# Performance work log

Measured on AMD Instinct MI355X. Metric: run time of the kernel, lower is better.

## Reference

```python
import jax, jax.numpy as jnp
import numpy as np
import math

N_QUBITS = 6
N_LAYERS = 3
OUT_DIM = 8
B = 131072
F = 24


def _gate_rx(a):
    # RX(a) = [[cos(a/2), -i sin(a/2)], [-i sin(a/2), cos(a/2)]]; a: scalar or [B]
    c = jnp.cos(a / 2).astype(jnp.complex64)
    s = (-1j * jnp.sin(a / 2)).astype(jnp.complex64)
    return jnp.stack([jnp.stack([c, s], -1), jnp.stack([s, c], -1)], -2)


def _gate_ry(a):
    c = jnp.cos(a / 2).astype(jnp.complex64)
    s = jnp.sin(a / 2).astype(jnp.complex64)
    return jnp.stack([jnp.stack([c, -s], -1), jnp.stack([s, c], -1)], -2)


def _gate_rz(a):
    # RZ(a) = diag(e^{-ia/2}, e^{ia/2})
    e = jnp.exp(-0.5j * a.astype(jnp.complex64))
    z = jnp.zeros_like(e)
    return jnp.stack([jnp.stack([e, z], -1), jnp.stack([z, jnp.conj(e)], -1)], -2)


def _apply_1q(state, gate, q, batched):
    # state: [B] + [2]*N_QUBITS ; gate: [2,2] or [B,2,2]
    s = jnp.moveaxis(state, 1 + q, 1)
    if batched:
        out = jnp.einsum('bij,bj...->bi...', gate, s)
    else:
        out = jnp.einsum('ij,bj...->bi...', gate, s)
    return jnp.moveaxis(out, 1, 1 + q)


def _apply_cnot(state, c, t):
    # flip target where control bit == 1
    cax = 1 + c
    s0 = jnp.take(state, 0, axis=cax)
    s1 = jnp.take(state, 1, axis=cax)
    tax = 1 + t if t < c else t  # control axis removed
    s1 = jnp.flip(s1, axis=tax)
    return jnp.stack([s0, s1], axis=cax)


def _circuit(x, theta):
    Bn = x.shape[0]
    # pooling branch of forward: chunks of size ceil(F/n_qubits)=4, mean each
    x_packed = x.reshape(Bn, N_QUBITS, F // N_QUBITS).mean(-1)
    angles = jnp.clip(x_packed, -6.0, 6.0) / 6.0 * math.pi  # [B, n_qubits]

    state = jnp.zeros((Bn,) + (2,) * N_QUBITS, dtype=jnp.complex64)
    state = state.at[(slice(None),) + (0,) * N_QUBITS].set(1.0)

    # angle encoding: RX(a_q), RZ(0.5*a_q) per qubit (batched gates)
    for q in range(N_QUBITS):
        state = _apply_1q(state, _gate_rx(angles[:, q]), q, batched=True)
        state = _apply_1q(state, _gate_rz(0.5 * angles[:, q]), q, batched=True)

    for l in range(N_LAYERS):
        for q in range(N_QUBITS - 1):
            state = _apply_cnot(state, q, q + 1)
        state = _apply_cnot(state, N_QUBITS - 1, 0)
        for q in range(N_QUBITS):
            state = _apply_1q(state, _gate_rx(theta[l, q, 0]), q, batched=False)
            state = _apply_1q(state, _gate_ry(theta[l, q, 1]), q, batched=False)
            state = _apply_1q(state, _gate_rz(theta[l, q, 2]), q, batched=False)

    probs = jnp.abs(state) ** 2  # real
    meas = []
    for k in range(OUT_DIM):
        q = k % N_QUBITS
        if k % 2 == 0:  # PauliZ
            pq = jnp.sum(probs, axis=tuple(a for a in range(1, N_QUBITS + 1) if a != 1 + q))
            meas.append(pq[:, 0] - pq[:, 1])
        else:  # PauliX: Re <psi| X_q |psi>
            flipped = jnp.flip(state, axis=1 + q)
            meas.append(jnp.real(jnp.sum(jnp.conj(state) * flipped, axis=tuple(range(1, N_QUBITS + 1)))))
    return jnp.stack(meas, axis=1).astype(jnp.float32)  # [B, out_dim]


def setup_inputs() -> dict:
    key = jax.random.key(0)
    k1, k2 = jax.random.split(key)
    x = jax.random.normal(k1, (B, F), dtype=jnp.float32)
    theta = jax.random.normal(k2, (N_LAYERS, N_QUBITS, 3), dtype=jnp.float32) * 0.1
    return {"x": x, "theta": theta}


def reference(x, theta):
    return _circuit(x, theta)
```

## Files before the change

### kernel.cpp

```cpp
#include <hip/hip_runtime.h>
#include <math.h>


__device__ __forceinline__ float2 pk_cmul(float2 g, float2 a) {
    float2 t;
    asm("v_pk_mul_f32 %0, %1, %2 op_sel:[0,0] op_sel_hi:[0,1]"
        : "=v"(t) : "v"(g), "v"(a));
    asm("v_pk_fma_f32 %0, %1, %2, %0 op_sel:[1,1,0] op_sel_hi:[1,0,1] neg_lo:[1,0,0]"
        : "+v"(t) : "v"(g), "v"(a));
    return t;
}
__device__ __forceinline__ float2 pk_cmac(float2 acc, float2 g, float2 a) {
    asm("v_pk_fma_f32 %0, %1, %2, %0 op_sel:[0,0,0] op_sel_hi:[0,1,1]"
        : "+v"(acc) : "v"(g), "v"(a));
    asm("v_pk_fma_f32 %0, %1, %2, %0 op_sel:[1,1,0] op_sel_hi:[1,0,1] neg_lo:[1,0,0]"
        : "+v"(acc) : "v"(g), "v"(a));
    return acc;
}
__device__ __forceinline__ float2 pk_sqacc(float2 acc, float2 a) {
    asm("v_pk_fma_f32 %0, %1, %1, %0" : "+v"(acc) : "v"(a));
    return acc;
}
__device__ __forceinline__ float2 pk_macv(float2 acc, float2 a, float2 b) {
    asm("v_pk_fma_f32 %0, %1, %2, %0" : "+v"(acc) : "v"(a), "v"(b));
    return acc;
}

__device__ __forceinline__ float xpair(float v) {
    return __int_as_float(__builtin_amdgcn_mov_dpp(__float_as_int(v), 0xB1, 0xF, 0xF, true));
}
__device__ __forceinline__ float2 xpair2(float2 v) {
    return make_float2(xpair(v.x), xpair(v.y));
}

template<int M>
__device__ __forceinline__ void apply1q(float2* st, float2 g00, float2 g01,
                                        float2 g10, float2 g11) {
#pragma unroll
    for (int j = 0; j < 32; ++j) {
        if (j & M) continue;
        float2 a = st[j], b = st[j + M];
        float2 na = pk_cmul(g00, a); na = pk_cmac(na, g01, b);
        float2 nb = pk_cmul(g10, a); nb = pk_cmac(nb, g11, b);
        st[j] = na; st[j + M] = nb;
    }
}

template<int MC, int MT>
__device__ __forceinline__ void cnot(float2* st) {
#pragma unroll
    for (int j = 0; j < 32; ++j) {
        if ((j & MC) && !(j & MT)) {
            float2 tmp = st[j]; st[j] = st[j + MT]; st[j + MT] = tmp;
        }
    }
}

struct cf { float r, i; };
__device__ __forceinline__ cf scmul(cf a, cf b) {
    return { fmaf(a.r, b.r, -a.i * b.i), fmaf(a.r, b.i, a.i * b.r) };
}

__global__ __launch_bounds__(256, 2) void qsim_kernel(
    const float* __restrict__ x, const float* __restrict__ theta,
    float* __restrict__ out) {
    __shared__ float2 gs[18 * 4];
    const int t = threadIdx.x;
    if (t < 18) {
        const float* th = theta + t * 3;
        float sx, cx, sy, cy, sz, cz;
        __sincosf(0.5f * th[0], &sx, &cx);
        __sincosf(0.5f * th[1], &sy, &cy);
        __sincosf(0.5f * th[2], &sz, &cz);
        cf m00 = {  cy * cx,  sy * sx };
        cf m01 = { -sy * cx, -cy * sx };
        cf m10 = {  sy * cx, -cy * sx };
        cf m11 = {  cy * cx, -sy * sx };
        cf e0 = { cz, -sz }, e1 = { cz, sz };
        cf g00 = scmul(e0, m00), g01 = scmul(e0, m01);
        cf g10 = scmul(e1, m10), g11 = scmul(e1, m11);
        float2* o = gs + t * 4;
        o[0] = make_float2(g00.r, g00.i);
        o[1] = make_float2(g01.r, g01.i);
        o[2] = make_float2(g10.r, g10.i);
        o[3] = make_float2(g11.r, g11.i);
    }
    __syncthreads();

    const int tg = blockIdx.x * 256 + t;
    const int b  = tg >> 1;
    const bool pb = (tg & 1) != 0;

    const float4* xv = reinterpret_cast<const float4*>(x + (size_t)b * 24);

    float2 st[32];
#pragma unroll
    for (int q = 0; q < 6; ++q) {
        float4 v = xv[q];
        float m = (v.x + v.y + v.z + v.w) * 0.25f;
        m = fminf(fmaxf(m, -6.0f), 6.0f);
        float a = m * 0.52359877559829887308f;
        float s2, c2, s4, c4;
        __sincosf(0.50f * a, &s2, &c2);
        __sincosf(0.25f * a, &s4, &c4);
        float2 v0 = make_float2(c4 * c2, -s4 * c2);
        float2 v1 = make_float2(s4 * s2, -c4 * s2);
        if (q == 0) {
            st[0] = pb ? v1 : v0;
        } else {
            const int mq = 32 >> q;
#pragma unroll
            for (int i = 0; i < 32; i += 2 * mq) {
                st[i + mq] = pk_cmul(st[i], v1);
                st[i]      = pk_cmul(st[i], v0);
            }
        }
    }

#pragma unroll 1
    for (int l = 0; l < 3; ++l) {
#pragma unroll
        for (int j = 0; j < 16; ++j) {
            float2 lo = st[j], hi = st[j + 16];
            st[j].x      = pb ? hi.x : lo.x;  st[j].y      = pb ? hi.y : lo.y;
            st[j + 16].x = pb ? lo.x : hi.x;  st[j + 16].y = pb ? lo.y : hi.y;
        }
        cnot<16, 8>(st);
        cnot< 8, 4>(st);
        cnot< 4, 2>(st);
        cnot< 2, 1>(st);
#pragma unroll
        for (int j = 1; j < 32; j += 2) st[j] = xpair2(st[j]);

        const float2* g = gs + l * 24;

        {
            float2 q00 = g[0], q01 = g[1], q10 = g[2], q11 = g[3];
            float2 gm, go;
            gm.x = pb ? q11.x : q00.x;  gm.y = pb ? q11.y : q00.y;
            go.x = pb ? q10.x : q01.x;  go.y = pb ? q10.y : q01.y;
#pragma unroll
            for (int j = 0; j < 32; ++j) {
                float2 other = xpair2(st[j]);
                float2 nv = pk_cmul(gm, st[j]);
                st[j] = pk_cmac(nv, go, other);
            }
        }
        apply1q<16>(st, g[ 4], g[ 5], g[ 6], g[ 7]);
        apply1q< 8>(st, g[ 8], g[ 9], g[10], g[11]);
        apply1q< 4>(st, g[12], g[13], g[14], g[15]);
        apply1q< 2>(st, g[16], g[17], g[18], g[19]);
        apply1q< 1>(st, g[20], g[21], g[22], g[23]);
    }

    float2 ps[4];
#pragma unroll
    for (int k = 0; k < 4; ++k) ps[k] = make_float2(0.f, 0.f);
#pragma unroll
    for (int j = 0; j < 32; ++j) {
        const int gi = (((j >> 3) & 1) << 1) | ((j >> 1) & 1);
        ps[gi] = pk_sqacc(ps[gi], st[j]);
    }
    float s[4];
#pragma unroll
    for (int k = 0; k < 4; ++k) s[k] = ps[k].x + ps[k].y;
    float tot = (s[0] + s[1]) + (s[2] + s[3]);
    float z0 = pb ? -tot : tot;
    float z2 = (s[0] + s[1]) - (s[2] + s[3]);
    float z4 = (s[0] + s[2]) - (s[1] + s[3]);

    float2 xa = make_float2(0.f, 0.f), xb = xa, xc = xa;
#pragma unroll
    for (int j = 0; j < 32; ++j) {
        if (!(j & 16)) xa = pk_macv(xa, st[j], st[j + 16]);
        if (!(j &  4)) xb = pk_macv(xb, st[j], st[j +  4]);
        if (!(j &  1)) xc = pk_macv(xc, st[j], st[j +  1]);
    }
    float x1 = xa.x + xa.y;
    float x3 = xb.x + xb.y;
    float x5 = xc.x + xc.y;

    z0 += xpair(z0); z2 += xpair(z2); z4 += xpair(z4);
    x1 += xpair(x1); x3 += xpair(x3); x5 += xpair(x5);
    x1 *= 2.f; x3 *= 2.f; x5 *= 2.f;

    float oa = pb ? z4 : z0;
    float ob = pb ? x5 : x1;
    float oc = pb ? z0 : z2;
    float od = pb ? x1 : x3;
    float4* ov = reinterpret_cast<float4*>(out + (size_t)b * 8);
    ov[pb ? 1 : 0] = make_float4(oa, ob, oc, od);
}

extern "C" void kernel_launch(void* const* d_in, const int* in_sizes, int n_in,
                              void* d_out, int out_size, void* d_ws, size_t ws_size,
                              hipStream_t stream) {
    const float* x     = (const float*)d_in[0];
    const float* theta = (const float*)d_in[1];
    float* out = (float*)d_out;
    const int B = in_sizes[0] / 24;
    qsim_kernel<<<dim3((B * 2) / 256), dim3(256), 0, stream>>>(x, theta, out);
}
```

Baseline: 88.05 us.

## Precompute circuit unitary and apply it to product states via split-fp16 MFMA

Since the variational layers are input-independent, a one-block kernel builds the full 64x64 complex circuit unitary as a 128x128 real matrix in workspace. The main kernel builds each sample's product-state encoding and multiplies it by the unitary using f16 MFMA instructions, splitting values into hi/lo halves to recover near-fp32 accuracy. This replaces the per-sample gate-by-gate VALU simulation with dense matrix-core work, at the cost of an extra launch, a workspace round-trip, and three MFMAs per tile.

```diff
diff --git a/kernel.cpp b/kernel.cpp
--- a/kernel.cpp
+++ b/kernel.cpp
@@ -1,6 +1,10 @@
 #include <hip/hip_runtime.h>
 #include <math.h>
 
+
+typedef _Float16 half8v __attribute__((ext_vector_type(8)));
+typedef _Float16 half4v __attribute__((ext_vector_type(4)));
+typedef float    float4v __attribute__((ext_vector_type(4)));
 
 __device__ __forceinline__ float2 pk_cmul(float2 g, float2 a) {
     float2 t;
@@ -17,14 +21,6 @@
         : "+v"(acc) : "v"(g), "v"(a));
     return acc;
 }
-__device__ __forceinline__ float2 pk_sqacc(float2 acc, float2 a) {
-    asm("v_pk_fma_f32 %0, %1, %1, %0" : "+v"(acc) : "v"(a));
-    return acc;
-}
-__device__ __forceinline__ float2 pk_macv(float2 acc, float2 a, float2 b) {
-    asm("v_pk_fma_f32 %0, %1, %2, %0" : "+v"(acc) : "v"(a), "v"(b));
-    return acc;
-}
 
 __device__ __forceinline__ float xpair(float v) {
     return __int_as_float(__builtin_amdgcn_mov_dpp(__float_as_int(v), 0xB1, 0xF, 0xF, true));
@@ -61,9 +57,12 @@
     return { fmaf(a.r, b.r, -a.i * b.i), fmaf(a.r, b.i, a.i * b.r) };
 }
 
-__global__ __launch_bounds__(256, 2) void qsim_kernel(
-    const float* __restrict__ x, const float* __restrict__ theta,
-    float* __restrict__ out) {
+__device__ __forceinline__ int rpos(int row, int k) {
+    return ((((row >> 4) * 4 + (k >> 5)) * 4 + ((k >> 3) & 3)) * 16 + (row & 15)) * 8 + (k & 7);
+}
+
+__global__ __launch_bounds__(128) void ubuild_kernel(
+    const float* __restrict__ theta, float* __restrict__ Rw) {
     __shared__ float2 gs[18 * 4];
     const int t = threadIdx.x;
     if (t < 18) {
@@ -87,109 +86,182 @@
     }
     __syncthreads();
 
-    const int tg = blockIdx.x * 256 + t;
-    const int b  = tg >> 1;
-    const bool pb = (tg & 1) != 0;
-
-    const float4* xv = reinterpret_cast<const float4*>(x + (size_t)b * 24);
+    const int c  = t >> 1;
+    const bool pb = (t & 1) != 0;
 
     float2 st[32];
 #pragma unroll
+    for (int j = 0; j < 32; ++j) st[j] = make_float2(0.f, 0.f);
+    if ((c >> 5) == (pb ? 1 : 0)) st[c & 31] = make_float2(1.f, 0.f);
+
+#pragma unroll 1
+    for (int l = 0; l < 3; ++l) {
+#pragma unroll
+        for (int j = 0; j < 16; ++j) {
+            float2 lo = st[j], hi = st[j + 16];
+            st[j].x      = pb ? hi.x : lo.x;  st[j].y      = pb ? hi.y : lo.y;
+            st[j + 16].x = pb ? lo.x : hi.x;  st[j + 16].y = pb ? lo.y : hi.y;
+        }
+        cnot<16, 8>(st);
+        cnot< 8, 4>(st);
+        cnot< 4, 2>(st);
+        cnot< 2, 1>(st);
+#pragma unroll
+        for (int j = 1; j < 32; j += 2) st[j] = xpair2(st[j]);
+
+        const float2* g = gs + l * 24;
+        {
+            float2 q00 = g[0], q01 = g[1], q10 = g[2], q11 = g[3];
+            float2 gm, go;
+            gm.x = pb ? q11.x : q00.x;  gm.y = pb ? q11.y : q00.y;
+            go.x = pb ? q10.x : q01.x;  go.y = pb ? q10.y : q01.y;
+#pragma unroll
+            for (int j = 0; j < 32; ++j) {
+                float2 other = xpair2(st[j]);
+                float2 nv = pk_cmul(gm, st[j]);
+                st[j] = pk_cmac(nv, go, other);
+            }
+        }
+        apply1q<16>(st, g[ 4], g[ 5], g[ 6], g[ 7]);
+        apply1q< 8>(st, g[ 8], g[ 9], g[10], g[11]);
+        apply1q< 4>(st, g[12], g[13], g[14], g[15]);
+        apply1q< 2>(st, g[16], g[17], g[18], g[19]);
+        apply1q< 1>(st, g[20], g[21], g[22], g[23]);
+    }
+
+#pragma unroll
+    for (int j = 0; j < 32; ++j) {
+        const int a = (pb ? 32 : 0) + j;
+        const float re = st[j].x, im = st[j].y;
+        Rw[rpos(a,      c)]      =  re;
+        Rw[rpos(a,      c + 64)] = -im;
+        Rw[rpos(a + 64, c)]      =  im;
+        Rw[rpos(a + 64, c + 64)] =  re;
+    }
+}
+
+__global__ __launch_bounds__(512) void qsim2_kernel(
+    const float* __restrict__ x, const float* __restrict__ Rg,
+    float* __restrict__ out) {
+    __shared__ __align__(16) _Float16 A[2][16384];
+    const int t = threadIdx.x;
+
+#pragma unroll
+    for (int ii = 0; ii < 8; ++ii) {
+        const int idx = ii * 2048 + t * 4;
+        float4 v = *reinterpret_cast<const float4*>(Rg + idx);
+        half4v hi, lo;
+        hi[0] = (_Float16)v.x; lo[0] = (_Float16)(v.x - (float)hi[0]);
+        hi[1] = (_Float16)v.y; lo[1] = (_Float16)(v.y - (float)hi[1]);
+        hi[2] = (_Float16)v.z; lo[2] = (_Float16)(v.z - (float)hi[2]);
+        hi[3] = (_Float16)v.w; lo[3] = (_Float16)(v.w - (float)hi[3]);
+        *reinterpret_cast<half4v*>(&A[0][idx]) = hi;
+        *reinterpret_cast<half4v*>(&A[1][idx]) = lo;
+    }
+    __syncthreads();
+
+    const int l = t & 63, w = t >> 6;
+    const int e16 = l & 15, h = l >> 4;
+    const int elem = (blockIdx.x * 8 + w) * 16 + e16;
+
+    const float4* xv = reinterpret_cast<const float4*>(x + (size_t)elem * 24);
+    float2 v0[6], v1[6];
+#pragma unroll
     for (int q = 0; q < 6; ++q) {
-        float4 v = xv[q];
-        float m = (v.x + v.y + v.z + v.w) * 0.25f;
+        float4 xq = xv[q];
+        float m = (xq.x + xq.y + xq.z + xq.w) * 0.25f;
         m = fminf(fmaxf(m, -6.0f), 6.0f);
         float a = m * 0.52359877559829887308f;
         float s2, c2, s4, c4;
         __sincosf(0.50f * a, &s2, &c2);
         __sincosf(0.25f * a, &s4, &c4);
-        float2 v0 = make_float2(c4 * c2, -s4 * c2);
-        float2 v1 = make_float2(s4 * s2, -c4 * s2);
-        if (q == 0) {
-            st[0] = pb ? v1 : v0;
-        } else {
-            const int mq = 32 >> q;
-#pragma unroll
-            for (int i = 0; i < 32; i += 2 * mq) {
-                st[i + mq] = pk_cmul(st[i], v1);
-                st[i]      = pk_cmul(st[i], v0);
-            }
-        }
-    }
-
-#pragma unroll 1
-    for (int l = 0; l < 3; ++l) {
-#pragma unroll
-        for (int j = 0; j < 16; ++j) {
-            float2 lo = st[j], hi = st[j + 16];
-            st[j].x      = pb ? hi.x : lo.x;  st[j].y      = pb ? hi.y : lo.y;
-            st[j + 16].x = pb ? lo.x : hi.x;  st[j + 16].y = pb ? lo.y : hi.y;
-        }
-        cnot<16, 8>(st);
-        cnot< 8, 4>(st);
-        cnot< 4, 2>(st);
-        cnot< 2, 1>(st);
-#pragma unroll
-        for (int j = 1; j < 32; j += 2) st[j] = xpair2(st[j]);
-
-        const float2* g = gs + l * 24;
-
-        {
-            float2 q00 = g[0], q01 = g[1], q10 = g[2], q11 = g[3];
-            float2 gm, go;
-            gm.x = pb ? q11.x : q00.x;  gm.y = pb ? q11.y : q00.y;
-            go.x = pb ? q10.x : q01.x;  go.y = pb ? q10.y : q01.y;
-#pragma unroll
-            for (int j = 0; j < 32; ++j) {
-                float2 other = xpair2(st[j]);
-                float2 nv = pk_cmul(gm, st[j]);
-                st[j] = pk_cmac(nv, go, other);
-            }
-        }
-        apply1q<16>(st, g[ 4], g[ 5], g[ 6], g[ 7]);
-        apply1q< 8>(st, g[ 8], g[ 9], g[10], g[11]);
-        apply1q< 4>(st, g[12], g[13], g[14], g[15]);
-        apply1q< 2>(st, g[16], g[17], g[18], g[19]);
-        apply1q< 1>(st, g[20], g[21], g[22], g[23]);
-    }
-
-    float2 ps[4];
-#pragma unroll
-    for (int k = 0; k < 4; ++k) ps[k] = make_float2(0.f, 0.f);
-#pragma unroll
-    for (int j = 0; j < 32; ++j) {
-        const int gi = (((j >> 3) & 1) << 1) | ((j >> 1) & 1);
-        ps[gi] = pk_sqacc(ps[gi], st[j]);
-    }
-    float s[4];
-#pragma unroll
-    for (int k = 0; k < 4; ++k) s[k] = ps[k].x + ps[k].y;
-    float tot = (s[0] + s[1]) + (s[2] + s[3]);
-    float z0 = pb ? -tot : tot;
-    float z2 = (s[0] + s[1]) - (s[2] + s[3]);
-    float z4 = (s[0] + s[2]) - (s[1] + s[3]);
-
-    float2 xa = make_float2(0.f, 0.f), xb = xa, xc = xa;
-#pragma unroll
-    for (int j = 0; j < 32; ++j) {
-        if (!(j & 16)) xa = pk_macv(xa, st[j], st[j + 16]);
-        if (!(j &  4)) xb = pk_macv(xb, st[j], st[j +  4]);
-        if (!(j &  1)) xc = pk_macv(xc, st[j], st[j +  1]);
-    }
-    float x1 = xa.x + xa.y;
-    float x3 = xb.x + xb.y;
-    float x5 = xc.x + xc.y;
-
-    z0 += xpair(z0); z2 += xpair(z2); z4 += xpair(z4);
-    x1 += xpair(x1); x3 += xpair(x3); x5 += xpair(x5);
-    x1 *= 2.f; x3 *= 2.f; x5 *= 2.f;
-
-    float oa = pb ? z4 : z0;
-    float ob = pb ? x5 : x1;
-    float oc = pb ? z0 : z2;
-    float od = pb ? x1 : x3;
-    float4* ov = reinterpret_cast<float4*>(out + (size_t)b * 8);
-    ov[pb ? 1 : 0] = make_float4(oa, ob, oc, od);
+        v0[q] = make_float2(c4 * c2, -s4 * c2);
+        v1[q] = make_float2(s4 * s2, -c4 * s2);
+    }
+    float2 u01[4], T[8];
+    u01[0] = pk_cmul(v0[4], v0[5]);
+    u01[1] = pk_cmul(v0[4], v1[5]);
+    u01[2] = pk_cmul(v1[4], v0[5]);
+    u01[3] = pk_cmul(v1[4], v1[5]);
+#pragma unroll
+    for (int j = 0; j < 8; ++j)
+        T[j] = pk_cmul((j & 4) ? v1[3] : v0[3], u01[j & 3]);
+    float2 Q  = pk_cmul((h & 2) ? v1[1] : v0[1], (h & 1) ? v1[2] : v0[2]);
+    float2 P1 = pk_cmul(v0[0], Q);
+    float2 P2 = pk_cmul(v1[0], Q);
+
+    half8v bhi[4], blo[4];
+#pragma unroll
+    for (int j = 0; j < 8; ++j) {
+        float2 a1 = pk_cmul(P1, T[j]);
+        float2 a2 = pk_cmul(P2, T[j]);
+        { _Float16 hh = (_Float16)a1.x; bhi[0][j] = hh; blo[0][j] = (_Float16)(a1.x - (float)hh); }
+        { _Float16 hh = (_Float16)a2.x; bhi[1][j] = hh; blo[1][j] = (_Float16)(a2.x - (float)hh); }
+        { _Float16 hh = (_Float16)a1.y; bhi[2][j] = hh; blo[2][j] = (_Float16)(a1.y - (float)hh); }
+        { _Float16 hh = (_Float16)a2.y; bhi[3][j] = hh; blo[3][j] = (_Float16)(a2.y - (float)hh); }
+    }
+
+    float4v acc[8];
+#pragma unroll
+    for (int m = 0; m < 8; ++m) acc[m] = (float4v){0.f, 0.f, 0.f, 0.f};
+#pragma unroll
+    for (int m = 0; m < 8; ++m) {
+#pragma unroll
+        for (int s = 0; s < 4; ++s) {
+            const int fo = ((m * 4 + s) * 64 + l) * 8;
+            half8v ah = *reinterpret_cast<const half8v*>(&A[0][fo]);
+            half8v al = *reinterpret_cast<const half8v*>(&A[1][fo]);
+            acc[m] = __builtin_amdgcn_mfma_f32_16x16x32_f16(ah, bhi[s], acc[m], 0, 0, 0);
+            acc[m] = __builtin_amdgcn_mfma_f32_16x16x32_f16(ah, blo[s], acc[m], 0, 0, 0);
+            acc[m] = __builtin_amdgcn_mfma_f32_16x16x32_f16(al, bhi[s], acc[m], 0, 0, 0);
+        }
+    }
+
+    float z0 = 0.f, z2 = 0.f, z4 = 0.f, x1 = 0.f, x3 = 0.f, x5 = 0.f;
+#pragma unroll
+    for (int m = 0; m < 4; ++m)
+#pragma unroll
+        for (int r = 0; r < 4; ++r) {
+            float re = acc[m][r], im = acc[m + 4][r];
+            float p = fmaf(re, re, im * im);
+            z0 += (m < 2) ? p : -p;
+            z2 += p;
+            z4 += (r < 2) ? p : -p;
+        }
+#pragma unroll
+    for (int m = 0; m < 4; m += 2)
+#pragma unroll
+        for (int r = 0; r < 4; ++r)
+            x1 += fmaf(acc[m][r], acc[m + 1][r], acc[m + 4][r] * acc[m + 5][r]);
+#pragma unroll
+    for (int m = 0; m < 4; ++m)
+#pragma unroll
+        for (int r = 0; r < 4; r += 2)
+            x5 += fmaf(acc[m][r], acc[m][r + 1], acc[m + 4][r] * acc[m + 4][r + 1]);
+#pragma unroll
+    for (int m = 0; m < 8; ++m)
+#pragma unroll
+        for (int r = 0; r < 4; ++r) {
+            float v = acc[m][r];
+            x3 = fmaf(v, __shfl_xor(v, 16, 64), x3);
+        }
+    if (h >= 2) z2 = -z2;
+
+#pragma unroll
+    for (int d = 16; d <= 32; d <<= 1) {
+        z0 += __shfl_xor(z0, d, 64);
+        z2 += __shfl_xor(z2, d, 64);
+        z4 += __shfl_xor(z4, d, 64);
+        x1 += __shfl_xor(x1, d, 64);
+        x3 += __shfl_xor(x3, d, 64);
+        x5 += __shfl_xor(x5, d, 64);
+    }
+    x1 *= 2.f; x5 *= 2.f;
+
+    if (h == 0)
+        *reinterpret_cast<float4*>(out + (size_t)elem * 8) = make_float4(z0, x1, z2, x3);
+    else if (h == 1)
+        *reinterpret_cast<float4*>(out + (size_t)elem * 8 + 4) = make_float4(z4, x5, z0, x1);
 }
 
 extern "C" void kernel_launch(void* const* d_in, const int* in_sizes, int n_in,
@@ -198,6 +270,8 @@
     const float* x     = (const float*)d_in[0];
     const float* theta = (const float*)d_in[1];
     float* out = (float*)d_out;
+    float* R   = (float*)d_ws;
     const int B = in_sizes[0] / 24;
-    qsim_kernel<<<dim3((B * 2) / 256), dim3(256), 0, stream>>>(x, theta, out);
-}
+    ubuild_kernel<<<dim3(1), dim3(128), 0, stream>>>(theta, R);
+    qsim2_kernel<<<dim3(B / 128), dim3(512), 0, stream>>>(x, R, out);
+}
```

New measurement: 149.9 us. +70.2%, slower.
